# Performance work log

Measured on AMD Instinct MI355X. Metric: run time of the kernel, lower is better.

Reference implementation:

```python
import jax, jax.numpy as jnp
import numpy as np

D_BRICK = 512  # args.brick_vector_dimension
H = 512        # hidden width


def setup_inputs() -> dict:
    key = jax.random.key(0)
    ks = jax.random.split(key, 20)
    B, N = 4, 192

    def w(k, shape, fan_in):
        return jax.random.uniform(k, shape, jnp.float32, -1.0, 1.0) / np.sqrt(fan_in)

    return {
        "brick_vectors": jax.random.normal(ks[0], (B, N, D_BRICK), jnp.float32),
        "xy": jax.random.uniform(ks[1], (B, N, 2), jnp.float32),
        # linear_xy: 2 -> 512
        "W_xy": w(ks[2], (H, 2), 2), "b_xy": w(ks[3], (H,), 2),
        # linear_a: D -> 512
        "W_a": w(ks[4], (H, D_BRICK), D_BRICK), "b_a": w(ks[5], (H,), D_BRICK),
        # linear_b: 512 -> 512
        "W_b": w(ks[6], (H, H), H), "b_b": w(ks[7], (H,), H),
        # combination_a: 1024 -> 512
        "W_ca": w(ks[8], (H, 2 * H), 2 * H), "b_ca": w(ks[9], (H,), 2 * H),
        # combination_b: 512 -> 512
        "W_cb": w(ks[10], (H, H), H), "b_cb": w(ks[11], (H,), H),
        # combination_c: 512 -> 512
        "W_cc": w(ks[12], (H, H), H), "b_cc": w(ks[13], (H,), H),
        # edge_out: 512 -> 2
        "W_out": w(ks[14], (2, H), H), "b_out": w(ks[15], (2,), H),
    }


def reference(brick_vectors, xy, W_xy, b_xy, W_a, b_a, W_b, b_b,
              W_ca, b_ca, W_cb, b_cb, W_cc, b_cc, W_out, b_out):
    # per-brick feature MLP: (B, N, 512)
    f = jnp.einsum('bnd,hd->bnh', brick_vectors, W_a) + b_a \
        + jnp.einsum('bnt,ht->bnh', xy, W_xy) + b_xy
    f = jax.nn.relu(f)
    f = jax.nn.relu(jnp.einsum('bnh,gh->bng', f, W_b) + b_b)

    # combination_a on concat(f[b,j], f[b,i]) without materializing the
    # (B, N, N, 1024) tensor: split the weight into the two 512 halves.
    # edge[b,i,j] = cat(features_a, features_b) where features_a = f[b,j]
    # (expanded over dim 1) and features_b = f[b,i] (expanded over dim 2).
    W1, W2 = W_ca[:, :H], W_ca[:, H:]
    u = jnp.einsum('bnh,gh->bng', f, W1)  # contribution from f[b, j]
    v = jnp.einsum('bnh,gh->bng', f, W2)  # contribution from f[b, i]
    e = jax.nn.relu(u[:, None, :, :] + v[:, :, None, :] + b_ca)  # (B,N,N,512)

    e = jax.nn.relu(jnp.einsum('bijh,gh->bijg', e, W_cb) + b_cb)
    e = jax.nn.relu(jnp.einsum('bijh,gh->bijg', e, W_cc) + b_cc)
    return jnp.einsum('bijh,oh->bijo', e, W_out) + b_out  # (B, N, N, 2)
```

## Files before the change

### kernel.cpp

```cpp
#include <hip/hip_runtime.h>


typedef short  short8  __attribute__((ext_vector_type(8)));
typedef short  short4v __attribute__((ext_vector_type(4)));
typedef float  f32x4   __attribute__((ext_vector_type(4)));

#define LDSW 520

__device__ inline unsigned short f2bf(float x) {
  unsigned u = __float_as_uint(x);
  unsigned r = (u + 0x7FFFu + ((u >> 16) & 1u)) >> 16;
  return (unsigned short)r;
}

template <int MT, int NT>
__device__ inline void zero_acc(f32x4 (&acc)[MT][NT]) {
#pragma unroll
  for (int mt = 0; mt < MT; ++mt)
#pragma unroll
    for (int nt = 0; nt < NT; ++nt) {
      f32x4 z = {0.f, 0.f, 0.f, 0.f};
      acc[mt][nt] = z;
    }
}

template <int MT, int NT>
__device__ inline void gemm_kloop(const short* E, const short* __restrict__ W,
                                  int lane, int nbase, f32x4 (&acc)[MT][NT]) {
  const int mrow = lane & 15, kg = lane >> 4;
  const short* El = E + mrow * LDSW + kg * 8;
  const short* Wl = W + (nbase + mrow) * 512 + kg * 8;
  short8 wF[2][NT];
#pragma unroll
  for (int nt = 0; nt < NT; ++nt) wF[0][nt] = *(const short8*)(Wl + nt * 16 * 512);
#pragma unroll
  for (int ks = 0; ks < 16; ++ks) {
    const int cur = ks & 1, nxt = cur ^ 1;
    if (ks < 15) {
      const int k1 = (ks + 1) * 32;
#pragma unroll
      for (int nt = 0; nt < NT; ++nt)
        wF[nxt][nt] = *(const short8*)(Wl + nt * 16 * 512 + k1);
    }
    const int k0 = ks * 32;
    short8 e0 = *(const short8*)(El + k0);
#pragma unroll
    for (int mt = 0; mt < MT; ++mt) {
      const short8 ecur = e0;
      if (mt < MT - 1) e0 = *(const short8*)(El + (mt + 1) * 16 * LDSW + k0);
#pragma unroll
      for (int nt = 0; nt < NT; ++nt)
        acc[mt][nt] = __builtin_amdgcn_mfma_f32_16x16x32_bf16(
            wF[cur][nt], ecur, acc[mt][nt], 0, 0, 0);
    }
  }
}

template <int MT, int NT>
__device__ inline void store_relu_lds(short* E, const float* __restrict__ bias,
                                      int lane, int nbase, f32x4 (&acc)[MT][NT]) {
  const int mrow = lane & 15, kg = lane >> 4;
#pragma unroll
  for (int nt = 0; nt < NT; ++nt) {
    const int oc = nbase + nt * 16 + kg * 4;
    const float4 bs = *(const float4*)(bias + oc);
#pragma unroll
    for (int mt = 0; mt < MT; ++mt) {
      short4v s;
      s.x = (short)f2bf(fmaxf(acc[mt][nt][0] + bs.x, 0.f));
      s.y = (short)f2bf(fmaxf(acc[mt][nt][1] + bs.y, 0.f));
      s.z = (short)f2bf(fmaxf(acc[mt][nt][2] + bs.z, 0.f));
      s.w = (short)f2bf(fmaxf(acc[mt][nt][3] + bs.w, 0.f));
      *(short4v*)&E[(mt * 16 + mrow) * LDSW + oc] = s;
    }
  }
}

__global__ void prep_kernel(const float* __restrict__ Wa, const float* __restrict__ Wb,
                            const float* __restrict__ Wca, const float* __restrict__ Wcb,
                            const float* __restrict__ Wcc, const float* __restrict__ Wout,
                            short* __restrict__ outS) {
  const int tid = blockIdx.x * blockDim.x + threadIdx.x;
  const int stride = gridDim.x * blockDim.x;
  const int M = 262144;
  for (int i = tid; i < 6 * M + 1024; i += stride) {
    float x;
    if (i < M) x = Wa[i];
    else if (i < 2 * M) x = Wb[i - M];
    else if (i < 3 * M) { const int t = i - 2 * M; x = Wca[(t >> 9) * 1024 + (t & 511)]; }
    else if (i < 4 * M) { const int t = i - 3 * M; x = Wca[(t >> 9) * 1024 + 512 + (t & 511)]; }
    else if (i < 5 * M) x = Wcb[i - 4 * M];
    else if (i < 6 * M) x = Wcc[i - 5 * M];
    else x = Wout[i - 6 * M];
    outS[i] = (short)f2bf(x);
  }
}

template <int MODE>
__global__ __launch_bounds__(256, 4) void node_layer(
    const void* __restrict__ Xin, const short* __restrict__ W,
    const float* __restrict__ bias, const float* __restrict__ xy,
    const float* __restrict__ Wxy, const float* __restrict__ bxy,
    void* __restrict__ Yout, float* __restrict__ vout, int colTiles) {
  __shared__ short X[64 * LDSW];
  __shared__ float xyl[128];
  const int tid = threadIdx.x, lane = tid & 63, wave = tid >> 6;
  const int rt = blockIdx.x / colTiles, ct = blockIdx.x % colTiles;
  const int row0 = rt * 64, c0 = ct * 64;

  if (MODE == 1) {
    const float* bv = (const float*)Xin;
    const int hc = (tid & 127) * 4, m0 = tid >> 7;
    for (int m = m0; m < 64; m += 2) {
      const float4 t = *(const float4*)(bv + (row0 + m) * 512 + hc);
      short4v s;
      s.x = (short)f2bf(t.x); s.y = (short)f2bf(t.y);
      s.z = (short)f2bf(t.z); s.w = (short)f2bf(t.w);
      *(short4v*)&X[m * LDSW + hc] = s;
    }
    if (tid < 128) xyl[tid] = xy[row0 * 2 + tid];
  } else {
    const short* xb = (const short*)Xin;
    const int hc = (tid & 63) * 8, m0 = tid >> 6;
    for (int m = m0; m < 64; m += 4)
      *(short8*)&X[m * LDSW + hc] = *(const short8*)(xb + (row0 + m) * 512 + hc);
  }
  __syncthreads();

  const int nbase = c0 + wave * 16;
  f32x4 acc[4][1];
  zero_acc<4, 1>(acc);
  gemm_kloop<4, 1>(X, W, lane, nbase, acc);

  const int mrow = lane & 15, kg = lane >> 4;
  const int oc = nbase + kg * 4;
  if (MODE == 3) {
    float* u = (float*)Yout;
#pragma unroll
    for (int mt = 0; mt < 4; ++mt) {
      const int row = row0 + mt * 16 + mrow;
      if (oc < 512) *(f32x4*)&u[row * 512 + oc] = acc[mt][0];
      else          *(f32x4*)&vout[row * 512 + oc - 512] = acc[mt][0];
    }
  } else {
    short* Y = (short*)Yout;
    const float4 bs = *(const float4*)(bias + oc);
    float b2[4] = {0.f, 0.f, 0.f, 0.f}, w0[4], w1[4];
    if (MODE == 1) {
      const float4 t = *(const float4*)(bxy + oc);
      b2[0] = t.x; b2[1] = t.y; b2[2] = t.z; b2[3] = t.w;
#pragma unroll
      for (int r = 0; r < 4; ++r) { w0[r] = Wxy[(oc + r) * 2]; w1[r] = Wxy[(oc + r) * 2 + 1]; }
    }
#pragma unroll
    for (int mt = 0; mt < 4; ++mt) {
      const int row = mt * 16 + mrow;
      short4v s;
#pragma unroll
      for (int r = 0; r < 4; ++r) {
        float xv = acc[mt][0][r] + ((const float*)&bs)[r];
        if (MODE == 1) xv += b2[r] + xyl[row * 2] * w0[r] + xyl[row * 2 + 1] * w1[r];
        ((short*)&s)[r] = (short)f2bf(fmaxf(xv, 0.f));
      }
      *(short4v*)&Y[(row0 + row) * 512 + oc] = s;
    }
  }
}

__global__ __launch_bounds__(512, 2) void edge_kernel(
    const float* __restrict__ u, const float* __restrict__ v,
    const short* __restrict__ Wcb, const short* __restrict__ Wcc,
    const short* __restrict__ Wout,
    const float* __restrict__ bca, const float* __restrict__ bcb,
    const float* __restrict__ bcc, const float* __restrict__ bout,
    float* __restrict__ out) {
  __shared__ short A[144 * LDSW];
  __shared__ float red[144 * 2 * 8];
  const int tid = threadIdx.x, lane = tid & 63, wave = tid >> 6;
  const int blk = blockIdx.x;
  const int b = blk >> 8, rem = blk & 255, ip = rem >> 2, jt = rem & 3;
  const float* urow0 = u + (b * 192 + jt * 48) * 512;
  const float* vrow0 = v + (b * 192 + ip * 3) * 512;

  {
    const int hc = (tid & 127) * 4, m0 = tid >> 7;
    const float4 v0 = *(const float4*)(vrow0 + hc);
    const float4 v1 = *(const float4*)(vrow0 + 512 + hc);
    const float4 v2 = *(const float4*)(vrow0 + 1024 + hc);
    const float4 bb = *(const float4*)(bca + hc);
#pragma unroll 4
    for (int m = m0; m < 144; m += 4) {
      const int ii = (m >= 96) ? 2 : (m >= 48 ? 1 : 0);
      const int jj = m - ii * 48;
      const float4 vv = (ii == 0) ? v0 : (ii == 1) ? v1 : v2;
      const float4 uu = *(const float4*)(urow0 + jj * 512 + hc);
      short4v s;
      s.x = (short)f2bf(fmaxf(uu.x + vv.x + bb.x, 0.f));
      s.y = (short)f2bf(fmaxf(uu.y + vv.y + bb.y, 0.f));
      s.z = (short)f2bf(fmaxf(uu.z + vv.z + bb.z, 0.f));
      s.w = (short)f2bf(fmaxf(uu.w + vv.w + bb.w, 0.f));
      *(short4v*)&A[m * LDSW + hc] = s;
    }
  }
  __syncthreads();

  const int nbase = wave * 64;
  f32x4 acc[9][4];

  zero_acc<9, 4>(acc);
  gemm_kloop<9, 4>(A, Wcb, lane, nbase, acc);
  __syncthreads();
  store_relu_lds<9, 4>(A, bcb, lane, nbase, acc);
  __syncthreads();

  zero_acc<9, 4>(acc);
  gemm_kloop<9, 4>(A, Wcc, lane, nbase, acc);
  __syncthreads();
  store_relu_lds<9, 4>(A, bcc, lane, nbase, acc);
  __syncthreads();

  f32x4 oacc[9];
#pragma unroll
  for (int mt = 0; mt < 9; ++mt) { f32x4 z = {0.f, 0.f, 0.f, 0.f}; oacc[mt] = z; }
  const int n = lane & 15, kg2 = lane >> 4;
#pragma unroll
  for (int kk = 0; kk < 2; ++kk) {
    const int k0 = wave * 64 + kk * 32 + kg2 * 8;
    short8 bf = {0, 0, 0, 0, 0, 0, 0, 0};
    if (n < 2) bf = *(const short8*)(Wout + n * 512 + k0);
#pragma unroll
    for (int mt = 0; mt < 9; ++mt) {
      const short8 af = *(const short8*)(A + (mt * 16 + n) * LDSW + k0);
      oacc[mt] = __builtin_amdgcn_mfma_f32_16x16x32_bf16(af, bf, oacc[mt], 0, 0, 0);
    }
  }
  if (n < 2) {
#pragma unroll
    for (int mt = 0; mt < 9; ++mt)
#pragma unroll
      for (int r = 0; r < 4; ++r) {
        const int row = mt * 16 + kg2 * 4 + r;
        red[(row * 2 + n) * 8 + wave] = oacc[mt][r];
      }
  }
  __syncthreads();
  if (tid < 288) {
    const int row = tid >> 1, o = tid & 1;
    float s = bout[o];
#pragma unroll
    for (int w = 0; w < 8; ++w) s += red[(row * 2 + o) * 8 + w];
    const int ii = (row >= 96) ? 2 : (row >= 48 ? 1 : 0);
    const int jj = row - ii * 48;
    out[((b * 192 + ip * 3 + ii) * 192 + jt * 48 + jj) * 2 + o] = s;
  }
}

extern "C" void kernel_launch(void* const* d_in, const int* in_sizes, int n_in,
                              void* d_out, int out_size, void* d_ws, size_t ws_size,
                              hipStream_t stream) {
  const float* bv   = (const float*)d_in[0];
  const float* xy   = (const float*)d_in[1];
  const float* Wxy  = (const float*)d_in[2];
  const float* bxy  = (const float*)d_in[3];
  const float* Wa   = (const float*)d_in[4];
  const float* ba   = (const float*)d_in[5];
  const float* Wb   = (const float*)d_in[6];
  const float* bb   = (const float*)d_in[7];
  const float* Wca  = (const float*)d_in[8];
  const float* bca  = (const float*)d_in[9];
  const float* Wcb  = (const float*)d_in[10];
  const float* bcb  = (const float*)d_in[11];
  const float* Wcc  = (const float*)d_in[12];
  const float* bcc  = (const float*)d_in[13];
  const float* Wout = (const float*)d_in[14];
  const float* bout = (const float*)d_in[15];
  float* out = (float*)d_out;

  short* S = (short*)d_ws;
  char* base = (char*)d_ws;
  short* WaB   = S;
  short* WbB   = S + 262144;
  short* WuvB  = S + 524288;
  short* WcbB  = S + 1048576;
  short* WccB  = S + 1310720;
  short* WoutB = S + 1572864;
  short* f1 = (short*)(base + 3147776);
  float* u  = (float*)(base + 3147776);
  short* f2 = (short*)(base + 4720640);
  float* v  = (float*)(base + 5507072);

  prep_kernel<<<512, 256, 0, stream>>>(Wa, Wb, Wca, Wcb, Wcc, Wout, S);
  node_layer<1><<<96, 256, 0, stream>>>(bv, WaB, ba, xy, Wxy, bxy, f1, nullptr, 8);
  node_layer<2><<<96, 256, 0, stream>>>(f1, WbB, bb, nullptr, nullptr, nullptr, f2, nullptr, 8);
  node_layer<3><<<192, 256, 0, stream>>>(f2, WuvB, nullptr, nullptr, nullptr, nullptr, u, v, 16);
  edge_kernel<<<1024, 512, 0, stream>>>(u, v, WcbB, WccB, WoutB, bca, bcb, bcc, bout, out);
}
```

Measured before the change: 295.0 us.

## Swizzle LDS tiles with XOR and pre-tile bf16 weights for coalesced fragment loads

Drops the padded LDS row stride (520) in favour of a 512-wide layout with an XOR swizzle of 8-element chunks by row, avoiding bank conflicts while shrinking LDS use. The weight prep kernel now writes weights in a 16x32 tiled order so each wave's MFMA fragment loads read contiguous 1KB blocks instead of strided rows. The prep kernel is also vectorised to 8 elements per thread. The cost is extra index arithmetic, and every LDS reader and writer must use the swizzle consistently.

```diff
diff --git a/kernel.cpp b/kernel.cpp
--- a/kernel.cpp
+++ b/kernel.cpp
@@ -4,8 +4,6 @@
 typedef short  short8  __attribute__((ext_vector_type(8)));
 typedef short  short4v __attribute__((ext_vector_type(4)));
 typedef float  f32x4   __attribute__((ext_vector_type(4)));
-
-#define LDSW 520
 
 __device__ inline unsigned short f2bf(float x) {
   unsigned u = __float_as_uint(x);
@@ -13,6 +11,10 @@
   return (unsigned short)r;
 }
 
+__device__ inline int lds_e(int row, int e) {
+  return row * 512 + ((((e >> 3) ^ (row & 7)) << 3) | (e & 7));
+}
+
 template <int MT, int NT>
 __device__ inline void zero_acc(f32x4 (&acc)[MT][NT]) {
 #pragma unroll
@@ -27,27 +29,27 @@
 template <int MT, int NT>
 __device__ inline void gemm_kloop(const short* E, const short* __restrict__ W,
                                   int lane, int nbase, f32x4 (&acc)[MT][NT]) {
-  const int mrow = lane & 15, kg = lane >> 4;
-  const short* El = E + mrow * LDSW + kg * 8;
-  const short* Wl = W + (nbase + mrow) * 512 + kg * 8;
+  const int mrow = lane & 15, kg = lane >> 4, xorv = mrow & 7;
+  const short* El = E + mrow * 512;
+  const short* Wl = W + (nbase >> 4) * 8192 + mrow * 32 + kg * 8;
   short8 wF[2][NT];
 #pragma unroll
-  for (int nt = 0; nt < NT; ++nt) wF[0][nt] = *(const short8*)(Wl + nt * 16 * 512);
+  for (int nt = 0; nt < NT; ++nt) wF[0][nt] = *(const short8*)(Wl + nt * 8192);
 #pragma unroll
   for (int ks = 0; ks < 16; ++ks) {
     const int cur = ks & 1, nxt = cur ^ 1;
     if (ks < 15) {
-      const int k1 = (ks + 1) * 32;
+      const int k1 = (ks + 1) * 512;
 #pragma unroll
       for (int nt = 0; nt < NT; ++nt)
-        wF[nxt][nt] = *(const short8*)(Wl + nt * 16 * 512 + k1);
-    }
-    const int k0 = ks * 32;
-    short8 e0 = *(const short8*)(El + k0);
+        wF[nxt][nt] = *(const short8*)(Wl + nt * 8192 + k1);
+    }
+    const int ch = ((ks * 4 + kg) ^ xorv) << 3;
+    short8 e0 = *(const short8*)(El + ch);
 #pragma unroll
     for (int mt = 0; mt < MT; ++mt) {
       const short8 ecur = e0;
-      if (mt < MT - 1) e0 = *(const short8*)(El + (mt + 1) * 16 * LDSW + k0);
+      if (mt < MT - 1) e0 = *(const short8*)(El + (mt + 1) * 8192 + ch);
 #pragma unroll
       for (int nt = 0; nt < NT; ++nt)
         acc[mt][nt] = __builtin_amdgcn_mfma_f32_16x16x32_bf16(
@@ -66,12 +68,13 @@
     const float4 bs = *(const float4*)(bias + oc);
 #pragma unroll
     for (int mt = 0; mt < MT; ++mt) {
+      const int row = mt * 16 + mrow;
       short4v s;
       s.x = (short)f2bf(fmaxf(acc[mt][nt][0] + bs.x, 0.f));
       s.y = (short)f2bf(fmaxf(acc[mt][nt][1] + bs.y, 0.f));
       s.z = (short)f2bf(fmaxf(acc[mt][nt][2] + bs.z, 0.f));
       s.w = (short)f2bf(fmaxf(acc[mt][nt][3] + bs.w, 0.f));
-      *(short4v*)&E[(mt * 16 + mrow) * LDSW + oc] = s;
+      *(short4v*)&E[lds_e(row, oc)] = s;
     }
   }
 }
@@ -83,16 +86,37 @@
   const int tid = blockIdx.x * blockDim.x + threadIdx.x;
   const int stride = gridDim.x * blockDim.x;
   const int M = 262144;
-  for (int i = tid; i < 6 * M + 1024; i += stride) {
-    float x;
-    if (i < M) x = Wa[i];
-    else if (i < 2 * M) x = Wb[i - M];
-    else if (i < 3 * M) { const int t = i - 2 * M; x = Wca[(t >> 9) * 1024 + (t & 511)]; }
-    else if (i < 4 * M) { const int t = i - 3 * M; x = Wca[(t >> 9) * 1024 + 512 + (t & 511)]; }
-    else if (i < 5 * M) x = Wcb[i - 4 * M];
-    else if (i < 6 * M) x = Wcc[i - 5 * M];
-    else x = Wout[i - 6 * M];
-    outS[i] = (short)f2bf(x);
+  const int NV = (6 * M + 1024) / 8;
+  for (int idx = tid; idx < NV; idx += stride) {
+    const int d0 = idx * 8;
+    const float* src;
+    if (d0 >= 6 * M) {
+      src = Wout + (d0 - 6 * M);
+    } else {
+      const int r = d0 / M;
+      if (r == 2 || r == 3) {
+        const int t = d0 - 2 * M;
+        const int tile = t >> 9, l = t & 511;
+        const int c = (tile >> 4) * 16 + (l >> 5);
+        const int k = (tile & 15) * 32 + (l & 31);
+        src = (c < 512) ? (Wca + c * 1024 + k) : (Wca + (c - 512) * 1024 + 512 + k);
+      } else {
+        const int t = d0 - r * M;
+        const int tile = t >> 9, l = t & 511;
+        const int c = (tile >> 4) * 16 + (l >> 5);
+        const int k = (tile & 15) * 32 + (l & 31);
+        const float* base = (r == 0) ? Wa : (r == 1) ? Wb : (r == 4) ? Wcb : Wcc;
+        src = base + c * 512 + k;
+      }
+    }
+    const float4 a = *(const float4*)src;
+    const float4 b = *(const float4*)(src + 4);
+    short8 s;
+    s[0] = (short)f2bf(a.x); s[1] = (short)f2bf(a.y);
+    s[2] = (short)f2bf(a.z); s[3] = (short)f2bf(a.w);
+    s[4] = (short)f2bf(b.x); s[5] = (short)f2bf(b.y);
+    s[6] = (short)f2bf(b.z); s[7] = (short)f2bf(b.w);
+    *(short8*)(outS + d0) = s;
   }
 }
 
@@ -102,7 +126,7 @@
     const float* __restrict__ bias, const float* __restrict__ xy,
     const float* __restrict__ Wxy, const float* __restrict__ bxy,
     void* __restrict__ Yout, float* __restrict__ vout, int colTiles) {
-  __shared__ short X[64 * LDSW];
+  __shared__ short X[64 * 512];
   __shared__ float xyl[128];
   const int tid = threadIdx.x, lane = tid & 63, wave = tid >> 6;
   const int rt = blockIdx.x / colTiles, ct = blockIdx.x % colTiles;
@@ -116,14 +140,14 @@
       short4v s;
       s.x = (short)f2bf(t.x); s.y = (short)f2bf(t.y);
       s.z = (short)f2bf(t.z); s.w = (short)f2bf(t.w);
-      *(short4v*)&X[m * LDSW + hc] = s;
+      *(short4v*)&X[lds_e(m, hc)] = s;
     }
     if (tid < 128) xyl[tid] = xy[row0 * 2 + tid];
   } else {
     const short* xb = (const short*)Xin;
     const int hc = (tid & 63) * 8, m0 = tid >> 6;
     for (int m = m0; m < 64; m += 4)
-      *(short8*)&X[m * LDSW + hc] = *(const short8*)(xb + (row0 + m) * 512 + hc);
+      *(short8*)&X[lds_e(m, hc)] = *(const short8*)(xb + (row0 + m) * 512 + hc);
   }
   __syncthreads();
 
@@ -174,7 +198,7 @@
     const float* __restrict__ bca, const float* __restrict__ bcb,
     const float* __restrict__ bcc, const float* __restrict__ bout,
     float* __restrict__ out) {
-  __shared__ short A[144 * LDSW];
+  __shared__ short A[144 * 512];
   __shared__ float red[144 * 2 * 8];
   const int tid = threadIdx.x, lane = tid & 63, wave = tid >> 6;
   const int blk = blockIdx.x;
@@ -199,7 +223,7 @@
       s.y = (short)f2bf(fmaxf(uu.y + vv.y + bb.y, 0.f));
       s.z = (short)f2bf(fmaxf(uu.z + vv.z + bb.z, 0.f));
       s.w = (short)f2bf(fmaxf(uu.w + vv.w + bb.w, 0.f));
-      *(short4v*)&A[m * LDSW + hc] = s;
+      *(short4v*)&A[lds_e(m, hc)] = s;
     }
   }
   __syncthreads();
@@ -222,25 +246,25 @@
   f32x4 oacc[9];
 #pragma unroll
   for (int mt = 0; mt < 9; ++mt) { f32x4 z = {0.f, 0.f, 0.f, 0.f}; oacc[mt] = z; }
-  const int n = lane & 15, kg2 = lane >> 4;
+  const int n2 = lane & 15, kg2 = lane >> 4;
 #pragma unroll
   for (int kk = 0; kk < 2; ++kk) {
-    const int k0 = wave * 64 + kk * 32 + kg2 * 8;
+    const int e = wave * 64 + kk * 32 + kg2 * 8;
     short8 bf = {0, 0, 0, 0, 0, 0, 0, 0};
-    if (n < 2) bf = *(const short8*)(Wout + n * 512 + k0);
+    if (n2 < 2) bf = *(const short8*)(Wout + n2 * 512 + e);
 #pragma unroll
     for (int mt = 0; mt < 9; ++mt) {
-      const short8 af = *(const short8*)(A + (mt * 16 + n) * LDSW + k0);
+      const short8 af = *(const short8*)&A[lds_e(mt * 16 + n2, e)];
       oacc[mt] = __builtin_amdgcn_mfma_f32_16x16x32_bf16(af, bf, oacc[mt], 0, 0, 0);
     }
   }
-  if (n < 2) {
+  if (n2 < 2) {
 #pragma unroll
     for (int mt = 0; mt < 9; ++mt)
 #pragma unroll
       for (int r = 0; r < 4; ++r) {
         const int row = mt * 16 + kg2 * 4 + r;
-        red[(row * 2 + n) * 8 + wave] = oacc[mt][r];
+        red[(row * 2 + n2) * 8 + wave] = oacc[mt][r];
       }
   }
   __syncthreads();
```

Result: slower. 335.3 us (+13.7%).
